# Kernel optimization log

Measured on AMD Instinct MI355X. Metric: run time of the kernel, lower is better.

Reference implementation:

```python
import jax, jax.numpy as jnp
import numpy as np

N_NODES = 100000
N_EDGES = 6_400_000
IN_DIM = 128


def gcn_conv(x, W, b, row, col, ew):
    """PyG GCNConv(normalize=True, add_self_loops=True) forward."""
    n = x.shape[0]
    loop = jnp.arange(n)
    row_sl = jnp.concatenate([row, loop])
    col_sl = jnp.concatenate([col, loop])
    ew_sl = jnp.concatenate([ew, jnp.ones((n,), ew.dtype)])
    # symmetric normalization: deg^{-1/2}[src] * w * deg^{-1/2}[dst]
    deg = jax.ops.segment_sum(ew_sl, col_sl, num_segments=n)
    safe_deg = jnp.where(deg > 0, deg, 1.0)
    dis = jnp.where(deg > 0, jax.lax.rsqrt(safe_deg), 0.0)
    norm = dis[row_sl] * ew_sl * dis[col_sl]
    h = x @ W  # [n, out_dim] linear transform first (small out_dim)
    # gather source features, scale, scatter-add into targets
    out = jax.ops.segment_sum(norm[:, None] * h[row_sl], col_sl, num_segments=n)
    return out + b


def setup_inputs() -> dict:
    key = jax.random.key(0)
    ks = jax.random.split(key, 12)
    X = jax.random.normal(ks[0], (N_NODES, IN_DIM), dtype=jnp.float32)
    edge_index = jax.random.randint(ks[1], (2, N_EDGES), 0, N_NODES, dtype=jnp.int64)
    edge_weight = jax.random.uniform(ks[2], (N_EDGES,), dtype=jnp.float32)

    def glorot(k, fan_in, fan_out):
        lim = np.sqrt(6.0 / (fan_in + fan_out)).astype(np.float32)
        return jax.random.uniform(k, (fan_in, fan_out), minval=-lim, maxval=lim, dtype=jnp.float32)

    return {
        "X": X,
        "edge_index": edge_index,
        "edge_weight": edge_weight,
        "W1": glorot(ks[3], IN_DIM, 12), "b1": jnp.zeros((12,), jnp.float32),
        "W2": glorot(ks[4], 12, 6), "b2": jnp.zeros((6,), jnp.float32),
        "W3": glorot(ks[5], 6, 3), "b3": jnp.zeros((3,), jnp.float32),
        "Wl": glorot(ks[6], 3, 1), "bl": jnp.zeros((1,), jnp.float32),
    }


def reference(X, edge_index, edge_weight, W1, b1, W2, b2, W3, b3, Wl, bl):
    row, col = edge_index[0], edge_index[1]
    h = jax.nn.relu(gcn_conv(X, W1, b1, row, col, edge_weight))
    # dropout p=0.2 is identity in eval mode
    h = jax.nn.relu(gcn_conv(h, W2, b2, row, col, edge_weight))
    h = jax.nn.relu(gcn_conv(h, W3, b3, row, col, edge_weight))
    out = jax.nn.sigmoid(h @ Wl + bl)
    return out.squeeze(1)  # [N]
```

## Files before the change

kernel.cpp:

```cpp
#include <hip/hip_runtime.h>
#include <cstdint>
#include <cstddef>

#define RANGE    128
#define RSHIFT   7
#define MAXBUCK  800
#define CSHIFT   12
#define CRANGE   4096
#define MAXC     32
#define FPB      32
#define CH_CNT   8192
#define CH_SC    4096
#define EPT      16
#define PAD      16
#define WSTR     132
#define STAGE_CAP 9216
#define SCAP     3072

typedef _Float16 h8 __attribute__((ext_vector_type(8)));

#define GLOAD_LDS16(gsrc, ldsb)                                                   \
    __builtin_amdgcn_global_load_lds(                                             \
        (const __attribute__((address_space(1))) uint32_t*)(gsrc),                \
        (__attribute__((address_space(3))) uint32_t*)(ldsb), 16, 0, 0)

static __device__ __forceinline__ unsigned pack_rec(int src, float w) {
    unsigned short hb = __builtin_bit_cast(unsigned short, (_Float16)w);
    return (unsigned)src | ((unsigned)hb << 17);
}
static __device__ __forceinline__ float rec_w(unsigned rec) {
    unsigned short hb = (unsigned short)(rec >> 17);
    return (float)__builtin_bit_cast(_Float16, hb);
}

__global__ void zero_pad_kernel(int* __restrict__ p, int n) {
    int i = blockIdx.x * blockDim.x + threadIdx.x;
    if (i < n) p[i * PAD] = 0;
}

__global__ void count_kernel(const int* __restrict__ col, int* __restrict__ fcnt,
                             int nfine, int E) {
    __shared__ int lcnt[MAXBUCK];
    int tid = threadIdx.x;
    for (int i = tid; i < nfine; i += blockDim.x) lcnt[i] = 0;
    __syncthreads();
    int base = blockIdx.x * CH_CNT;
    int end  = min(E, base + CH_CNT);
    for (int e = base + tid; e < end; e += blockDim.x)
        atomicAdd(&lcnt[col[e] >> RSHIFT], 1);
    __syncthreads();
    for (int i = tid; i < nfine; i += blockDim.x)
        if (lcnt[i]) atomicAdd(&fcnt[i * PAD], lcnt[i]);
}

__global__ void scan_kernel(const int* __restrict__ fcnt, int* __restrict__ fbase,
                            int* __restrict__ fcur, int* __restrict__ cbase,
                            int* __restrict__ ccur, int* __restrict__ row_ptr,
                            int nfine, int ncoarse, int N, int E) {
    __shared__ int lds[1024];
    int T = threadIdx.x;
    int s = (T < nfine) ? fcnt[T * PAD] : 0;
    lds[T] = s;
    __syncthreads();
    for (int off = 1; off < 1024; off <<= 1) {
        int v = (T >= off) ? lds[T - off] : 0;
        __syncthreads();
        lds[T] += v;
        __syncthreads();
    }
    int excl = lds[T] - s;
    if (T < nfine) { fbase[T] = excl; fcur[T * PAD] = excl; }
    if ((T & (FPB - 1)) == 0 && (T >> 5) < ncoarse) {
        cbase[T >> 5] = excl;
        ccur[(T >> 5) * PAD] = excl;
    }
    if (T == 0) { fbase[nfine] = E; cbase[ncoarse] = E; row_ptr[N] = E; }
}

__global__ void coarse_scatter_kernel(const int* __restrict__ row, const int* __restrict__ col,
                                      const float* __restrict__ ew, int* __restrict__ ccur,
                                      uint2* __restrict__ partA, int ncoarse, int E) {
    __shared__ uint2 stage[CH_SC];
    __shared__ unsigned char sb[CH_SC];
    __shared__ int lcnt[MAXC], lofs[MAXC], gofs[MAXC];
    __shared__ int total_s;
    int tid = threadIdx.x;
    if (tid < MAXC) lcnt[tid] = 0;
    __syncthreads();
    int base = blockIdx.x * CH_SC;
    int cnt  = min(E - base, CH_SC);

    uint2 rec[EPT]; int rnk[EPT]; int bb[EPT];
#pragma unroll
    for (int k = 0; k < EPT; k++) {
        int idx = tid + (k << 8);
        if (idx < cnt) {
            int e = base + idx;
            int c = col[e];
            int b = c >> CSHIFT;
            bb[k]  = b;
            rec[k] = make_uint2((unsigned)row[e] | ((unsigned)(c & (CRANGE - 1)) << 17),
                                __float_as_uint(ew[e]));
            rnk[k] = atomicAdd(&lcnt[b], 1);
        }
    }
    __syncthreads();
    if (tid == 0) {
        int run = 0;
        for (int i = 0; i < ncoarse; i++) { lofs[i] = run; run += lcnt[i]; }
        total_s = run;
    }
    __syncthreads();
    if (tid < ncoarse) {
        int c = lcnt[tid];
        if (c) {
            int g = atomicAdd(&ccur[tid * PAD], c);
            gofs[tid] = g - lofs[tid];
        }
    }
#pragma unroll
    for (int k = 0; k < EPT; k++) {
        int idx = tid + (k << 8);
        if (idx < cnt) {
            int p = lofs[bb[k]] + rnk[k];
            stage[p] = rec[k];
            sb[p] = (unsigned char)bb[k];
        }
    }
    __syncthreads();
    int total = total_s;
    for (int i = tid; i < total; i += 256)
        partA[gofs[sb[i]] + i] = stage[i];
}

__global__ __launch_bounds__(256, 3)
void fine_scatter_kernel(const uint2* __restrict__ partA, const int* __restrict__ cbase,
                                    int* __restrict__ fcur, uint2* __restrict__ partB,
                                    int nfine, int ncoarse, int E) {
    __shared__ uint2 stage[CH_SC];
    __shared__ unsigned short sb[CH_SC];
    __shared__ int lcnt[MAXBUCK], lofs[MAXBUCK], gofs[MAXBUCK];
    __shared__ int tmp[256];
    __shared__ int scb[MAXC + 1];
    __shared__ int rlo_s, total_s;
    int tid = threadIdx.x;
    int base = blockIdx.x * CH_SC;
    int cnt  = min(E - base, CH_SC);
    if (tid <= ncoarse) scb[tid] = cbase[tid];
    for (int i = tid; i < nfine; i += 256) lcnt[i] = 0;
    if (tid == 0) {
        int r = 0;
        while (r < ncoarse - 1 && cbase[r + 1] <= base) ++r;
        rlo_s = r;
    }
    __syncthreads();
    int rlo = rlo_s;

    uint2 rec[EPT]; int rnk[EPT]; int ff[EPT];
#pragma unroll
    for (int k = 0; k < EPT; k++) {
        int idx = tid + (k << 8);
        if (idx < cnt) {
            int e = base + idx;
            uint2 v = partA[e];
            int r = rlo;
            while (e >= scb[r + 1]) ++r;
            int col12 = (int)((v.x >> 17) & (CRANGE - 1));
            int f = (r << 5) | (col12 >> RSHIFT);
            ff[k]  = f;
            rec[k] = make_uint2((v.x & 0x1FFFFu) | ((unsigned)(col12 & (RANGE - 1)) << 17), v.y);
            rnk[k] = atomicAdd(&lcnt[f], 1);
        }
    }
    __syncthreads();
    {
        const int Cc = (nfine + 255) >> 8;
        int b0 = tid * Cc;
        int s = 0;
        for (int i = 0; i < Cc; i++) {
            int idx = b0 + i;
            if (idx < nfine) s += lcnt[idx];
        }
        tmp[tid] = s;
        __syncthreads();
        for (int off = 1; off < 256; off <<= 1) {
            int v = (tid >= off) ? tmp[tid - off] : 0;
            __syncthreads();
            tmp[tid] += v;
            __syncthreads();
        }
        int run = tmp[tid] - s;
        for (int i = 0; i < Cc; i++) {
            int idx = b0 + i;
            if (idx < nfine) { lofs[idx] = run; run += lcnt[idx]; }
        }
        if (tid == 255) total_s = tmp[255];
    }
    __syncthreads();
    for (int i = tid; i < nfine; i += 256) {
        int c = lcnt[i];
        if (c) {
            int g = atomicAdd(&fcur[i * PAD], c);
            gofs[i] = g - lofs[i];
        }
    }
#pragma unroll
    for (int k = 0; k < EPT; k++) {
        int idx = tid + (k << 8);
        if (idx < cnt) {
            int p = lofs[ff[k]] + rnk[k];
            stage[p] = rec[k];
            sb[p] = (unsigned short)ff[k];
        }
    }
    __syncthreads();
    int total = total_s;
    for (int i = tid; i < total; i += 256)
        partB[gofs[sb[i]] + i] = stage[i];
}

__global__ __launch_bounds__(512, 8)
void bucket_csr_kernel(const uint2* __restrict__ part, const int* __restrict__ bbase,
                       int* __restrict__ row_ptr, float* __restrict__ dis,
                       unsigned* __restrict__ csr, int N) {
    __shared__ unsigned cst[STAGE_CAP];
    __shared__ int   scnt[RANGE];
    __shared__ int   sscan[RANGE];
    __shared__ float sdeg[RANGE];
    __shared__ float sdis[RANGE];
    int b = blockIdx.x, tid = threadIdx.x;
    int s = bbase[b], t = bbase[b + 1];
    int cnt = t - s;
    if (tid < RANGE) { scnt[tid] = 0; sdeg[tid] = 1.0f; }
    __syncthreads();
    for (int i = tid; i < cnt; i += 512) {
        uint2 r = part[s + i];
        int c = (r.x >> 17) & (RANGE - 1);
        atomicAdd(&scnt[c], 1);
        atomicAdd(&sdeg[c], __uint_as_float(r.y));
    }
    __syncthreads();
    int cnt_t = 0;
    if (tid < RANGE) { cnt_t = scnt[tid]; sscan[tid] = cnt_t; }
    __syncthreads();
    for (int off = 1; off < RANGE; off <<= 1) {
        int v = 0;
        if (tid < RANGE && tid >= off) v = sscan[tid - off];
        __syncthreads();
        if (tid < RANGE) sscan[tid] += v;
        __syncthreads();
    }
    if (tid < RANGE) {
        int excl = sscan[tid] - cnt_t;
        int node = b * RANGE + tid;
        float dn = rsqrtf(sdeg[tid]);
        sdis[tid] = dn;
        if (node < N) {
            row_ptr[node] = s + excl;
            dis[node] = dn;
        }
        scnt[tid] = excl;
    }
    __syncthreads();
    for (int i = tid; i < cnt; i += 512) {
        uint2 r = part[s + i];
        int c   = (r.x >> 17) & (RANGE - 1);
        int src = (int)(r.x & 0x1FFFFu);
        float w = sdis[c] * __uint_as_float(r.y);
        unsigned rec = pack_rec(src, w);
        int p = atomicAdd(&scnt[c], 1);
        if (p < STAGE_CAP) cst[p] = rec;
        else               csr[s + p] = rec;
    }
    __syncthreads();
    int lim = min(cnt, STAGE_CAP);
    for (int i = tid; i < lim; i += 512)
        csr[s + i] = cst[i];
}

__global__ void lin1_kernel(const float* __restrict__ X, const float* __restrict__ W1,
                            const float* __restrict__ dis, uint4* __restrict__ t1, int n) {
    __shared__ float w1t[12 * WSTR];
    int tid = threadIdx.x;
    for (int i = tid; i < 128 * 12; i += 256) {
        int k = i / 12, o = i - k * 12;
        w1t[o * WSTR + k] = W1[i];
    }
    __syncthreads();
    int gt   = blockIdx.x * 256 + tid;
    int node = gt >> 3;
    int sub  = gt & 7;
    if (node >= n) return;

    const float4* xp = (const float4*)(X + (size_t)node * 128 + sub * 16);
    float4 x0 = xp[0], x1 = xp[1], x2 = xp[2], x3 = xp[3];

    float res[12];
#pragma unroll
    for (int o = 0; o < 12; o++) {
        const float4* wp = (const float4*)(w1t + o * WSTR + sub * 16);
        float4 w0 = wp[0], w1v = wp[1], w2 = wp[2], w3 = wp[3];
        float s;
        s  = x0.x * w0.x + x0.y * w0.y + x0.z * w0.z + x0.w * w0.w;
        s += x1.x * w1v.x + x1.y * w1v.y + x1.z * w1v.z + x1.w * w1v.w;
        s += x2.x * w2.x + x2.y * w2.y + x2.z * w2.z + x2.w * w2.w;
        s += x3.x * w3.x + x3.y * w3.y + x3.z * w3.z + x3.w * w3.w;
        res[o] = s;
    }
#pragma unroll
    for (int o = 0; o < 12; o++) {
        res[o] += __shfl_xor(res[o], 1, 64);
        res[o] += __shfl_xor(res[o], 2, 64);
        res[o] += __shfl_xor(res[o], 4, 64);
    }
    if (sub == 0) {
        h8 a, b;
#pragma unroll
        for (int o = 0; o < 8; o++) a[o] = (_Float16)res[o];
#pragma unroll
        for (int o = 0; o < 4; o++) b[o] = (_Float16)res[8 + o];
#pragma unroll
        for (int o = 4; o < 8; o++) b[o] = (_Float16)0.f;
        uint4 ua = __builtin_bit_cast(uint4, a);
        uint4 ub = __builtin_bit_cast(uint4, b);
        ub.z = __float_as_uint(dis[node]);
        ub.w = 0u;
        uint4* dst = t1 + (size_t)node * 2;
        dst[0] = ua;
        dst[1] = ub;
    }
}

template <int DIN, int ROWW, int DOUT, bool LAST>
__global__ __launch_bounds__(256)
void agg_kernel(const int* __restrict__ row_ptr, const unsigned* __restrict__ csr,
                const uint4* __restrict__ hin,
                const float* __restrict__ b_this, const float* __restrict__ W_next,
                const float* __restrict__ b_next, void* __restrict__ hout_v, int n) {
    __shared__ unsigned scsr[SCAP];
    int tid = threadIdx.x;
    int nodeBase = blockIdx.x << 5;
    int node = nodeBase + (tid >> 3);
    int sub  = tid & 7;
    int endNode  = min(nodeBase + 32, n);
    int blkStart = row_ptr[nodeBase];
    int blkEnd   = row_ptr[endNode];
    int blkCnt   = blkEnd - blkStart;
    int lim = min(blkCnt, SCAP);
    {
        int wave = tid >> 6, lane = tid & 63;
        int iters = (lim + 1023) >> 10;
        for (int it = 0; it < iters; ++it) {
            int recBase = (it << 10) + (wave << 8);
            const unsigned* src = csr + blkStart + recBase + (lane << 2);
            GLOAD_LDS16(src, (char*)scsr + ((size_t)recBase << 2));
        }
    }
    asm volatile("s_waitcnt vmcnt(0)" ::: "memory");
    __syncthreads();

    if (node >= n) return;
    int start = row_ptr[node];
    int end   = row_ptr[node + 1];
    float acc[DIN], acc2[DIN];
#pragma unroll
    for (int d = 0; d < DIN; d++) { acc[d] = 0.f; acc2[d] = 0.f; }

    auto body = [&](unsigned r, float* a_) {
        int src  = (int)(r & 0x1FFFFu);
        float wq = rec_w(r);
        const uint4* hr = hin + (size_t)src * ROWW;
        if constexpr (DIN == 12) {
            uint4 ua = hr[0], ub = hr[1];
            float norm = wq * __uint_as_float(ub.z);
            h8 a = __builtin_bit_cast(h8, ua);
            h8 b = __builtin_bit_cast(h8, ub);
#pragma unroll
            for (int d = 0; d < 8; d++) a_[d] += norm * (float)a[d];
#pragma unroll
            for (int d = 0; d < 4; d++) a_[8 + d] += norm * (float)b[d];
        } else if constexpr (DIN == 6) {
            uint4 u = hr[0];
            float norm = wq * __uint_as_float(u.w);
            h8 a = __builtin_bit_cast(h8, u);
#pragma unroll
            for (int d = 0; d < 6; d++) a_[d] += norm * (float)a[d];
        } else {
            uint4 u = hr[0];
            float norm = wq * __uint_as_float(u.z);
            h8 a = __builtin_bit_cast(h8, u);
#pragma unroll
            for (int d = 0; d < 3; d++) a_[d] += norm * (float)a[d];
        }
    };

    if (blkCnt <= SCAP) {
        int ls = start - blkStart;
        int le = end - blkStart;
        int e = ls + sub;
        for (; e + 8 < le; e += 16) {
            unsigned r0 = scsr[e];
            unsigned r1 = scsr[e + 8];
            body(r0, acc);
            body(r1, acc2);
        }
        if (e < le) body(scsr[e], acc);
    } else {
        int e = start + sub;
        for (; e + 8 < end; e += 16) {
            unsigned r0 = csr[e];
            unsigned r1 = csr[e + 8];
            body(r0, acc);
            body(r1, acc2);
        }
        if (e < end) body(csr[e], acc);
    }

#pragma unroll
    for (int d = 0; d < DIN; d++) {
        acc[d] += acc2[d];
        acc[d] += __shfl_xor(acc[d], 1, 64);
        acc[d] += __shfl_xor(acc[d], 2, 64);
        acc[d] += __shfl_xor(acc[d], 4, 64);
    }

    if (sub == 0) {
        const uint4* hn = hin + (size_t)node * ROWW;
        float v[DIN];
        float dn;
        if constexpr (DIN == 12) {
            uint4 ua = hn[0], ub = hn[1];
            dn = __uint_as_float(ub.z);
            float s2 = dn * dn;
            h8 a = __builtin_bit_cast(h8, ua);
            h8 b = __builtin_bit_cast(h8, ub);
#pragma unroll
            for (int d = 0; d < 8; d++) v[d] = fmaxf(acc[d] + s2 * (float)a[d] + b_this[d], 0.f);
#pragma unroll
            for (int d = 0; d < 4; d++) v[8 + d] = fmaxf(acc[8 + d] + s2 * (float)b[d] + b_this[8 + d], 0.f);
        } else if constexpr (DIN == 6) {
            uint4 u = hn[0];
            dn = __uint_as_float(u.w);
            float s2 = dn * dn;
            h8 a = __builtin_bit_cast(h8, u);
#pragma unroll
            for (int d = 0; d < 6; d++) v[d] = fmaxf(acc[d] + s2 * (float)a[d] + b_this[d], 0.f);
        } else {
            uint4 u = hn[0];
            dn = __uint_as_float(u.z);
            float s2 = dn * dn;
            h8 a = __builtin_bit_cast(h8, u);
#pragma unroll
            for (int d = 0; d < 3; d++) v[d] = fmaxf(acc[d] + s2 * (float)a[d] + b_this[d], 0.f);
        }
        if constexpr (!LAST) {
            float o[DOUT];
#pragma unroll
            for (int oo = 0; oo < DOUT; oo++) {
                float z = 0.f;
#pragma unroll
                for (int d = 0; d < DIN; d++) z += v[d] * W_next[d * DOUT + oo];
                o[oo] = z;
            }
            h8 w;
#pragma unroll
            for (int oo = 0; oo < 8; oo++) w[oo] = (_Float16)0.f;
#pragma unroll
            for (int oo = 0; oo < DOUT; oo++) w[oo] = (_Float16)o[oo];
            uint4 uw = __builtin_bit_cast(uint4, w);
            if constexpr (DOUT == 6) uw.w = __float_as_uint(dn);
            else                     uw.z = __float_as_uint(dn);
            ((uint4*)hout_v)[node] = uw;
        } else {
            float z = b_next[0];
#pragma unroll
            for (int d = 0; d < DIN; d++) z += v[d] * W_next[d];
            ((float*)hout_v)[node] = 1.0f / (1.0f + expf(-z));
        }
    }
}

extern "C" void kernel_launch(void* const* d_in, const int* in_sizes, int n_in,
                              void* d_out, int out_size, void* d_ws, size_t ws_size,
                              hipStream_t stream) {
    const float* X  = (const float*)d_in[0];
    const int*   ei = (const int*)d_in[1];
    const float* ew = (const float*)d_in[2];
    const float* W1 = (const float*)d_in[3];
    const float* b1 = (const float*)d_in[4];
    const float* W2 = (const float*)d_in[5];
    const float* b2 = (const float*)d_in[6];
    const float* W3 = (const float*)d_in[7];
    const float* b3 = (const float*)d_in[8];
    const float* Wl = (const float*)d_in[9];
    const float* bl = (const float*)d_in[10];
    float* out = (float*)d_out;

    const int N = in_sizes[0] / 128;
    const int E = in_sizes[1] / 2;
    const int* row = ei;
    const int* col = ei + E;
    const int nfine   = (N + RANGE - 1) >> RSHIFT;
    const int ncoarse = (N + CRANGE - 1) >> CSHIFT;

    char* ws = (char*)d_ws;
    size_t off = 0;
    auto carve = [&](size_t bytes) -> void* {
        void* p = ws + off;
        off += (bytes + 255) & ~(size_t)255;
        return p;
    };
    int*   fcnt    = (int*)  carve((size_t)MAXBUCK * PAD * 4);
    int*   fcur    = (int*)  carve((size_t)MAXBUCK * PAD * 4);
    int*   ccur    = (int*)  carve((size_t)MAXC * PAD * 4);
    int*   cbase   = (int*)  carve((size_t)(MAXC + 1) * 4);
    int*   fbase   = (int*)  carve((size_t)(MAXBUCK + 1) * 4);
    int*   row_ptr = (int*)  carve((size_t)(N + 1) * 4);
    float* dis     = (float*)carve((size_t)N * 4);
    uint2* partA   = (uint2*)carve((size_t)E * 8);
    uint2* partB   = (uint2*)carve((size_t)(E + STAGE_CAP) * 8);
    unsigned* csr = (unsigned*)partA;
    uint4* t1  = (uint4*)partB;
    uint4* t2  = t1 + (size_t)N * 2;
    uint4* t3  = t2 + (size_t)N;
    (void)ws_size; (void)n_in; (void)out_size;

    const int bCnt = (E + CH_CNT - 1) / CH_CNT;
    const int bSc  = (E + CH_SC - 1) / CH_SC;
    const int bL   = ((size_t)N * 8 + 255) / 256;
    const int bA   = (N + 31) / 32;

    zero_pad_kernel<<<(nfine + 255) / 256, 256, 0, stream>>>(fcnt, nfine);
    count_kernel<<<bCnt, 256, 0, stream>>>(col, fcnt, nfine, E);
    scan_kernel<<<1, 1024, 0, stream>>>(fcnt, fbase, fcur, cbase, ccur, row_ptr,
                                        nfine, ncoarse, N, E);
    coarse_scatter_kernel<<<bSc, 256, 0, stream>>>(row, col, ew, ccur, partA, ncoarse, E);
    fine_scatter_kernel<<<bSc, 256, 0, stream>>>(partA, cbase, fcur, partB, nfine, ncoarse, E);
    bucket_csr_kernel<<<nfine, 512, 0, stream>>>(partB, fbase, row_ptr, dis, csr, N);
    lin1_kernel<<<bL, 256, 0, stream>>>(X, W1, dis, t1, N);
    agg_kernel<12, 2, 6, false><<<bA, 256, 0, stream>>>(row_ptr, csr, t1, b1, W2, nullptr, t2, N);
    agg_kernel< 6, 1, 3, false><<<bA, 256, 0, stream>>>(row_ptr, csr, t2, b2, W3, nullptr, t3, N);
    agg_kernel< 3, 1, 1, true ><<<bA, 256, 0, stream>>>(row_ptr, csr, t3, b3, Wl, bl, out, N);
}
```

Baseline: 452.9 us.

## Defer destination normalization to aggregation and unroll edge loop four ways

The CSR build no longer multiplies each edge weight by the destination's deg^{-1/2}. The degree accumulation moves into the second pass, which removes one LDS atomic pass and the sdis table. The aggregation kernels now multiply the summed neighbour contribution by dn once per node. The shared-memory edge loop gets a four-accumulator unroll for more memory-level parallelism, and launch bounds request 4 blocks per CU, which risks register pressure with the extra accumulators.

```diff
diff --git a/kernel.cpp b/kernel.cpp
--- a/kernel.cpp
+++ b/kernel.cpp
@@ -227,7 +227,6 @@
     __shared__ int   scnt[RANGE];
     __shared__ int   sscan[RANGE];
     __shared__ float sdeg[RANGE];
-    __shared__ float sdis[RANGE];
     int b = blockIdx.x, tid = threadIdx.x;
     int s = bbase[b], t = bbase[b + 1];
     int cnt = t - s;
@@ -237,7 +236,6 @@
         uint2 r = part[s + i];
         int c = (r.x >> 17) & (RANGE - 1);
         atomicAdd(&scnt[c], 1);
-        atomicAdd(&sdeg[c], __uint_as_float(r.y));
     }
     __syncthreads();
     int cnt_t = 0;
@@ -253,12 +251,7 @@
     if (tid < RANGE) {
         int excl = sscan[tid] - cnt_t;
         int node = b * RANGE + tid;
-        float dn = rsqrtf(sdeg[tid]);
-        sdis[tid] = dn;
-        if (node < N) {
-            row_ptr[node] = s + excl;
-            dis[node] = dn;
-        }
+        if (node < N) row_ptr[node] = s + excl;
         scnt[tid] = excl;
     }
     __syncthreads();
@@ -266,13 +259,18 @@
         uint2 r = part[s + i];
         int c   = (r.x >> 17) & (RANGE - 1);
         int src = (int)(r.x & 0x1FFFFu);
-        float w = sdis[c] * __uint_as_float(r.y);
+        float w = __uint_as_float(r.y);
+        atomicAdd(&sdeg[c], w);
         unsigned rec = pack_rec(src, w);
         int p = atomicAdd(&scnt[c], 1);
         if (p < STAGE_CAP) cst[p] = rec;
         else               csr[s + p] = rec;
     }
     __syncthreads();
+    if (tid < RANGE) {
+        int node = b * RANGE + tid;
+        if (node < N) dis[node] = rsqrtf(sdeg[tid]);
+    }
     int lim = min(cnt, STAGE_CAP);
     for (int i = tid; i < lim; i += 512)
         csr[s + i] = cst[i];
@@ -332,7 +330,7 @@
 }
 
 template <int DIN, int ROWW, int DOUT, bool LAST>
-__global__ __launch_bounds__(256)
+__global__ __launch_bounds__(256, 4)
 void agg_kernel(const int* __restrict__ row_ptr, const unsigned* __restrict__ csr,
                 const uint4* __restrict__ hin,
                 const float* __restrict__ b_this, const float* __restrict__ W_next,
@@ -362,9 +360,9 @@
     if (node >= n) return;
     int start = row_ptr[node];
     int end   = row_ptr[node + 1];
-    float acc[DIN], acc2[DIN];
-#pragma unroll
-    for (int d = 0; d < DIN; d++) { acc[d] = 0.f; acc2[d] = 0.f; }
+    float acc[DIN], acc2[DIN], acc3[DIN], acc4[DIN];
+#pragma unroll
+    for (int d = 0; d < DIN; d++) { acc[d] = 0.f; acc2[d] = 0.f; acc3[d] = 0.f; acc4[d] = 0.f; }
 
     auto body = [&](unsigned r, float* a_) {
         int src  = (int)(r & 0x1FFFFu);
@@ -398,11 +396,17 @@
         int ls = start - blkStart;
         int le = end - blkStart;
         int e = ls + sub;
+        for (; e + 24 < le; e += 32) {
+            unsigned r0 = scsr[e];
+            unsigned r1 = scsr[e + 8];
+            unsigned r2 = scsr[e + 16];
+            unsigned r3 = scsr[e + 24];
+            body(r0, acc); body(r1, acc2); body(r2, acc3); body(r3, acc4);
+        }
         for (; e + 8 < le; e += 16) {
             unsigned r0 = scsr[e];
             unsigned r1 = scsr[e + 8];
-            body(r0, acc);
-            body(r1, acc2);
+            body(r0, acc); body(r1, acc2);
         }
         if (e < le) body(scsr[e], acc);
     } else {
@@ -410,15 +414,14 @@
         for (; e + 8 < end; e += 16) {
             unsigned r0 = csr[e];
             unsigned r1 = csr[e + 8];
-            body(r0, acc);
-            body(r1, acc2);
+            body(r0, acc); body(r1, acc2);
         }
         if (e < end) body(csr[e], acc);
     }
 
 #pragma unroll
     for (int d = 0; d < DIN; d++) {
-        acc[d] += acc2[d];
+        acc[d] += acc2[d] + acc3[d] + acc4[d];
         acc[d] += __shfl_xor(acc[d], 1, 64);
         acc[d] += __shfl_xor(acc[d], 2, 64);
         acc[d] += __shfl_xor(acc[d], 4, 64);
@@ -435,23 +438,23 @@
             h8 a = __builtin_bit_cast(h8, ua);
             h8 b = __builtin_bit_cast(h8, ub);
 #pragma unroll
-            for (int d = 0; d < 8; d++) v[d] = fmaxf(acc[d] + s2 * (float)a[d] + b_this[d], 0.f);
-#pragma unroll
-            for (int d = 0; d < 4; d++) v[8 + d] = fmaxf(acc[8 + d] + s2 * (float)b[d] + b_this[8 + d], 0.f);
+            for (int d = 0; d < 8; d++) v[d] = fmaxf(dn * acc[d] + s2 * (float)a[d] + b_this[d], 0.f);
+#pragma unroll
+            for (int d = 0; d < 4; d++) v[8 + d] = fmaxf(dn * acc[8 + d] + s2 * (float)b[d] + b_this[8 + d], 0.f);
         } else if constexpr (DIN == 6) {
             uint4 u = hn[0];
             dn = __uint_as_float(u.w);
             float s2 = dn * dn;
             h8 a = __builtin_bit_cast(h8, u);
 #pragma unroll
-            for (int d = 0; d < 6; d++) v[d] = fmaxf(acc[d] + s2 * (float)a[d] + b_this[d], 0.f);
+            for (int d = 0; d < 6; d++) v[d] = fmaxf(dn * acc[d] + s2 * (float)a[d] + b_this[d], 0.f);
         } else {
             uint4 u = hn[0];
             dn = __uint_as_float(u.z);
             float s2 = dn * dn;
             h8 a = __builtin_bit_cast(h8, u);
 #pragma unroll
-            for (int d = 0; d < 3; d++) v[d] = fmaxf(acc[d] + s2 * (float)a[d] + b_this[d], 0.f);
+            for (int d = 0; d < 3; d++) v[d] = fmaxf(dn * acc[d] + s2 * (float)a[d] + b_this[d], 0.f);
         }
         if constexpr (!LAST) {
             float o[DOUT];
```

Result: slower. 464.7 us (+2.6%).
